# Kernel optimization log

Measured on AMD Instinct MI355X. Metric: run time of the kernel, lower is better.

## Reference

```python
import jax, jax.numpy as jnp
import numpy as np

SEQ, B, IN, H = 2048, 256, 64, 256


def setup_inputs() -> dict:
    key = jax.random.key(0)
    ks = jax.random.split(key, 5)
    s_in = 1.0 / np.sqrt(IN)
    s_h = 1.0 / np.sqrt(H)
    return {
        "x": jax.random.normal(ks[0], (SEQ, B, IN), jnp.float32),
        # combined gate weights, order (f, i, o, g)
        "Wx": jax.random.uniform(ks[1], (IN, 4 * H), jnp.float32, -s_in, s_in),
        "Wh": jax.random.uniform(ks[2], (H, 4 * H), jnp.float32, -s_h, s_h),
        "bx": jax.random.uniform(ks[3], (4 * H,), jnp.float32, -s_in, s_in),
        "bh": jax.random.uniform(ks[4], (4 * H,), jnp.float32, -s_h, s_h),
    }


def reference(x, Wx, Wh, bx, bh):
    # x: [T, B, IN]. Precompute input projections for all timesteps (one big GEMM).
    gx = jnp.einsum('tbi,ih->tbh', x, Wx) + bx + bh  # [T, B, 4H]
    h0 = jnp.zeros((x.shape[1], Wh.shape[0]), x.dtype)
    c0 = jnp.zeros_like(h0)

    def step(carry, gx_t):
        h, c = carry
        gates = gx_t + h @ Wh  # [B, 4H]
        f, i, o, g = jnp.split(gates, 4, axis=-1)
        c = jax.nn.sigmoid(f) * c + jax.nn.sigmoid(i) * jnp.tanh(g)
        h = jax.nn.sigmoid(o) * jnp.tanh(c)
        return (h, c), h

    (h, c), h_seq = jax.lax.scan(step, (h0, c0), gx)
    return h_seq, h, c
```

## Files before the change

kernel.cpp:

```cpp
#include <hip/hip_runtime.h>


#define T_SEQ 2048
#define B_SZ  256
#define IN_SZ 64
#define H_SZ  256
#define G4    1024
#define NKF   10
#define NCT   64
#define LDSK  648
#define FRAG_BYTES (NCT * NKF * 64 * 16)
#define BIAS_OFF   FRAG_BYTES
#define FLAGS_OFF  (FRAG_BYTES + 4096)
#define XBUF_OFF   (FRAG_BYTES + 8192)

typedef float f32x4 __attribute__((ext_vector_type(4)));
typedef short s16x8 __attribute__((ext_vector_type(8)));
typedef short s16x2 __attribute__((ext_vector_type(2)));
typedef unsigned u32x4 __attribute__((ext_vector_type(4)));

__device__ __forceinline__ short f2bf(float f) {
    unsigned u = __builtin_bit_cast(unsigned, f);
    u = u + 0x7fffu + ((u >> 16) & 1u);
    return (short)(u >> 16);
}
__device__ __forceinline__ float bf2f(short s) {
    return __builtin_bit_cast(float, ((unsigned)(unsigned short)s) << 16);
}
__device__ __forceinline__ float fsigmoid(float v) {
    return __builtin_amdgcn_rcpf(1.0f + __expf(-v));
}
__device__ __forceinline__ float ftanh(float v) {
    return 2.0f * __builtin_amdgcn_rcpf(1.0f + __expf(-2.0f * v)) - 1.0f;
}

__global__ void repack_kernel(const float* __restrict__ Wx,
                              const float* __restrict__ Wh,
                              const float* __restrict__ bx,
                              const float* __restrict__ bh,
                              s16x8* __restrict__ fragbuf,
                              float* __restrict__ bias) {
    const int blk  = blockIdx.x;
    const int lane = threadIdx.x;
    const int ct = blk / NKF;
    const int kf = blk - ct * NKF;
    const int n  = ct * 16 + (lane & 15);
    const int q  = lane >> 4;
    s16x8 frag;
#pragma unroll
    for (int j = 0; j < 8; ++j) {
        const int k = kf * 32 + q * 8 + j;
        const float v = (k < IN_SZ) ? Wx[k * G4 + n] : Wh[(k - IN_SZ) * G4 + n];
        frag[j] = f2bf(v);
    }
    fragbuf[blk * 64 + lane] = frag;
    if (blk < 16) {
        const int i = blk * 64 + lane;
        bias[i] = bx[i] + bh[i];
    }
}

__global__ void init_flags(unsigned* __restrict__ flags) {
    if (threadIdx.x < 32) flags[threadIdx.x] = 0u;
}

__global__ __launch_bounds__(512, 2) void lstm_persist(
        const float* __restrict__ x,
        const s16x8* __restrict__ fragbuf,
        const float* __restrict__ bias,
        float* __restrict__ out,
        unsigned* __restrict__ flags,
        unsigned* __restrict__ xbuf) {
    __shared__ short lds_a[2 * 16 * LDSK];

    const int tid  = threadIdx.x;
    const int lane = tid & 63;
    const int w    = tid >> 6;
    const int q    = lane >> 4;
    const int ln   = lane & 15;
    const int bid  = blockIdx.x;
    const int g    = bid >> 1;
    const int p    = bid & 1;
    const int peer = bid ^ 1;
    const int S    = g * 16;
    const int hb   = p * 8 + w;
    const int col  = hb * 16 + ln;

    for (int i = tid; i < 2 * 16 * LDSK; i += 512) lds_a[i] = 0;

    s16x8 wt[4][10];
#pragma unroll
    for (int ci = 0; ci < 4; ++ci) {
        const int ct = ci * 16 + hb;
#pragma unroll
        for (int j = 0; j < 10; ++j) {
            const int kf = (j < 2) ? j
                         : (j < 6 ? 2 + 4 * p + (j - 2)
                                  : 2 + 4 * (1 - p) + (j - 6));
            wt[ci][j] = fragbuf[(size_t)(ct * NKF + kf) * 64 + lane];
        }
    }
    float bs[4];
#pragma unroll
    for (int ci = 0; ci < 4; ++ci) bs[ci] = bias[(ci * 16 + hb) * 16 + ln];

    f32x4 cs = {0.f, 0.f, 0.f, 0.f};

    const int xrow = tid >> 5;
    const int xi   = (tid & 31) << 1;
    const float* xp0 = x + (size_t)(S + xrow) * IN_SZ + xi;
    float xv0 = xp0[0], xv1 = xp0[1];

    __syncthreads();

    for (int t = 0; t < T_SEQ; ++t) {
        const int cur = t & 1;
        short* L  = lds_a + cur * (16 * LDSK);
        short* Ln = lds_a + (1 - cur) * (16 * LDSK);

        {
            const short h0 = f2bf(xv0), h1 = f2bf(xv1);
            const short l0 = f2bf(xv0 - bf2f(h0));
            const short l1 = f2bf(xv1 - bf2f(h1));
            s16x2 hv = {h0, h1}, lv = {l0, l1};
            *reinterpret_cast<s16x2*>(&L[xrow * LDSK + xi])       = hv;
            *reinterpret_cast<s16x2*>(&L[xrow * LDSK + 320 + xi]) = lv;
        }
        {
            const int tn = (t + 1 < T_SEQ) ? t + 1 : t;
            const float* xp = xp0 + (size_t)tn * (B_SZ * IN_SZ);
            xv0 = xp[0]; xv1 = xp[1];
        }

        if (t > 0) {
            while (__hip_atomic_load(&flags[peer], __ATOMIC_RELAXED,
                                     __HIP_MEMORY_SCOPE_AGENT) < (unsigned)t) {
                __builtin_amdgcn_s_sleep(1);
            }
            __builtin_amdgcn_fence(__ATOMIC_ACQUIRE, "agent");
            const u32x4* ps = (const u32x4*)(xbuf
                              + (size_t)(peer * 2 + ((t - 1) & 1)) * 2048);
            const u32x4 v = ps[tid];
            const int colp = tid >> 2;
            const int cg   = 128 * (1 - p) + colp;
            const int m0   = (tid & 3) * 4;
#pragma unroll
            for (int e = 0; e < 4; ++e) {
                const unsigned u = v[e];
                const int m = m0 + e;
                L[m * LDSK + 64  + cg] = (short)(u & 0xffffu);
                L[m * LDSK + 384 + cg] = (short)(u >> 16);
            }
        }
        __syncthreads();

        f32x4 acc[4], acl[4];
#pragma unroll
        for (int ci = 0; ci < 4; ++ci) {
            acc[ci] = (f32x4){bs[ci], bs[ci], bs[ci], bs[ci]};
            acl[ci] = (f32x4){0.f, 0.f, 0.f, 0.f};
        }
#pragma unroll
        for (int j = 0; j < 10; ++j) {
            const int kf = (j < 2) ? j
                         : (j < 6 ? 2 + 4 * p + (j - 2)
                                  : 2 + 4 * (1 - p) + (j - 6));
            const s16x8 ah = *reinterpret_cast<const s16x8*>(
                                 &L[ln * LDSK + kf * 32 + q * 8]);
            const s16x8 al = *reinterpret_cast<const s16x8*>(
                                 &L[ln * LDSK + 320 + kf * 32 + q * 8]);
#pragma unroll
            for (int ci = 0; ci < 4; ++ci) {
                acc[ci] = __builtin_amdgcn_mfma_f32_16x16x32_bf16(ah, wt[ci][j], acc[ci], 0, 0, 0);
                acl[ci] = __builtin_amdgcn_mfma_f32_16x16x32_bf16(al, wt[ci][j], acl[ci], 0, 0, 0);
            }
        }
#pragma unroll
        for (int ci = 0; ci < 4; ++ci) acc[ci] += acl[ci];

        float* hs = out + (size_t)t * (B_SZ * H_SZ) + (size_t)S * H_SZ;
        unsigned* os = xbuf + (size_t)(bid * 2 + cur) * 2048;
        const bool last = (t == T_SEQ - 1);
        unsigned pu[4];
#pragma unroll
        for (int r = 0; r < 4; ++r) {
            const float fv = fsigmoid(acc[0][r]);
            const float iv = fsigmoid(acc[1][r]);
            const float ov = fsigmoid(acc[2][r]);
            const float gv = ftanh(acc[3][r]);
            const float cf = fv * cs[r] + iv * gv;
            cs[r] = cf;
            const float hv = ov * ftanh(cf);
            const int m = q * 4 + r;
            __builtin_nontemporal_store(hv, hs + m * H_SZ + col);
            const short hh = f2bf(hv);
            const short hl = f2bf(hv - bf2f(hh));
            Ln[m * LDSK + 64  + col] = hh;
            Ln[m * LDSK + 384 + col] = hl;
            pu[r] = ((unsigned)(unsigned short)hh)
                  | (((unsigned)(unsigned short)hl) << 16);
            if (last) {
                float* fin = out + (size_t)T_SEQ * B_SZ * H_SZ;
                fin[(S + m) * H_SZ + col] = hv;
                fin[B_SZ * H_SZ + (S + m) * H_SZ + col] = cf;
            }
        }
        {
            const int colp = w * 16 + ln;
            unsigned long long* od =
                (unsigned long long*)(os + colp * 16 + q * 4);
            const unsigned long long u01 =
                (unsigned long long)pu[0] | ((unsigned long long)pu[1] << 32);
            const unsigned long long u23 =
                (unsigned long long)pu[2] | ((unsigned long long)pu[3] << 32);
            __hip_atomic_store(&od[0], u01, __ATOMIC_RELAXED,
                               __HIP_MEMORY_SCOPE_AGENT);
            __hip_atomic_store(&od[1], u23, __ATOMIC_RELAXED,
                               __HIP_MEMORY_SCOPE_AGENT);
        }
        __syncthreads();
        if (tid == 0)
            __hip_atomic_store(&flags[bid], (unsigned)(t + 1),
                               __ATOMIC_RELEASE, __HIP_MEMORY_SCOPE_AGENT);
    }
}

extern "C" void kernel_launch(void* const* d_in, const int* in_sizes, int n_in,
                              void* d_out, int out_size, void* d_ws, size_t ws_size,
                              hipStream_t stream) {
    const float* x  = (const float*)d_in[0];
    const float* Wx = (const float*)d_in[1];
    const float* Wh = (const float*)d_in[2];
    const float* bx = (const float*)d_in[3];
    const float* bh = (const float*)d_in[4];
    float* out = (float*)d_out;

    s16x8*    fragbuf = (s16x8*)d_ws;
    float*    bias    = (float*)((char*)d_ws + BIAS_OFF);
    unsigned* flags   = (unsigned*)((char*)d_ws + FLAGS_OFF);
    unsigned* xbuf    = (unsigned*)((char*)d_ws + XBUF_OFF);

    repack_kernel<<<NCT * NKF, 64, 0, stream>>>(Wx, Wh, bx, bh, fragbuf, bias);
    init_flags<<<1, 64, 0, stream>>>(flags);
    lstm_persist<<<32, 512, 0, stream>>>(x, fragbuf, bias, out, flags, xbuf);
}
```

Measured before the change: 12.57 ms.

## Overlap peer hidden-state exchange with local MFMA work using per-wave flags

Restructures the per-timestep cross-block exchange. Each wave publishes its h slice in MFMA-fragment layout and bumps a per-wave counter with fetch_add, so the peer can load those fragments straight into registers instead of going through LDS plus a barrier. The local K-fragments (x and own-half h) are computed before waiting on the peer, so the wait overlaps with MFMA work. The LDS layout switches to an XOR swizzle to avoid bank conflicts, and the x staging for step t+1 moves to the end of step t. The relaxed loads after the spin and the counter-based readiness check rely on subtle memory-ordering assumptions, which is a correctness risk.

```diff
diff --git a/kernel.cpp b/kernel.cpp
--- a/kernel.cpp
+++ b/kernel.cpp
@@ -8,16 +8,19 @@
 #define G4    1024
 #define NKF   10
 #define NCT   64
-#define LDSK  648
 #define FRAG_BYTES (NCT * NKF * 64 * 16)
 #define BIAS_OFF   FRAG_BYTES
 #define FLAGS_OFF  (FRAG_BYTES + 4096)
 #define XBUF_OFF   (FRAG_BYTES + 8192)
+#define ROW_B   768
+#define BUF_B   (16 * ROW_B)
+#define PUB_OFF (2 * BUF_B)
 
 typedef float f32x4 __attribute__((ext_vector_type(4)));
 typedef short s16x8 __attribute__((ext_vector_type(8)));
 typedef short s16x2 __attribute__((ext_vector_type(2)));
-typedef unsigned u32x4 __attribute__((ext_vector_type(4)));
+typedef unsigned long long u64;
+typedef u64 u64x2 __attribute__((ext_vector_type(2)));
 
 __device__ __forceinline__ short f2bf(float f) {
     unsigned u = __builtin_bit_cast(unsigned, f);
@@ -32,6 +35,9 @@
 }
 __device__ __forceinline__ float ftanh(float v) {
     return 2.0f * __builtin_amdgcn_rcpf(1.0f + __expf(-2.0f * v)) - 1.0f;
+}
+__device__ __forceinline__ short* aptr(char* lds, int buf, int row, int off) {
+    return (short*)(lds + buf * BUF_B + row * ROW_B + (off ^ ((row & 7) << 4)));
 }
 
 __global__ void repack_kernel(const float* __restrict__ Wx,
@@ -70,8 +76,8 @@
         const float* __restrict__ bias,
         float* __restrict__ out,
         unsigned* __restrict__ flags,
-        unsigned* __restrict__ xbuf) {
-    __shared__ short lds_a[2 * 16 * LDSK];
+        char* __restrict__ xbuf) {
+    __shared__ char lds[PUB_OFF + 8704];
 
     const int tid  = threadIdx.x;
     const int lane = tid & 63;
@@ -85,8 +91,10 @@
     const int S    = g * 16;
     const int hb   = p * 8 + w;
     const int col  = hb * 16 + ln;
-
-    for (int i = tid; i < 2 * 16 * LDSK; i += 512) lds_a[i] = 0;
+    const int colp = w * 16 + ln;
+
+    for (int i = tid; i < (PUB_OFF + 8704) / 4; i += 512)
+        ((int*)lds)[i] = 0;
 
     s16x8 wt[4][10];
 #pragma unroll
@@ -111,48 +119,40 @@
     const float* xp0 = x + (size_t)(S + xrow) * IN_SZ + xi;
     float xv0 = xp0[0], xv1 = xp0[1];
 
+    {
+        const short h0 = f2bf(xv0), h1 = f2bf(xv1);
+        const short l0 = f2bf(xv0 - bf2f(h0));
+        const short l1 = f2bf(xv1 - bf2f(h1));
+        *(s16x2*)aptr(lds, 0, xrow, xi * 2)       = (s16x2){h0, h1};
+        *(s16x2*)aptr(lds, 0, xrow, 384 + xi * 2) = (s16x2){l0, l1};
+    }
+    {
+        const float* xp = xp0 + (size_t)(B_SZ * IN_SZ);
+        xv0 = xp[0]; xv1 = xp[1];
+    }
+    unsigned* psw = (unsigned*)(lds + PUB_OFF) + w * 272;
+    unsigned rdyflag = 0;
+
     __syncthreads();
 
     for (int t = 0; t < T_SEQ; ++t) {
         const int cur = t & 1;
-        short* L  = lds_a + cur * (16 * LDSK);
-        short* Ln = lds_a + (1 - cur) * (16 * LDSK);
-
-        {
-            const short h0 = f2bf(xv0), h1 = f2bf(xv1);
-            const short l0 = f2bf(xv0 - bf2f(h0));
-            const short l1 = f2bf(xv1 - bf2f(h1));
-            s16x2 hv = {h0, h1}, lv = {l0, l1};
-            *reinterpret_cast<s16x2*>(&L[xrow * LDSK + xi])       = hv;
-            *reinterpret_cast<s16x2*>(&L[xrow * LDSK + 320 + xi]) = lv;
-        }
-        {
-            const int tn = (t + 1 < T_SEQ) ? t + 1 : t;
-            const float* xp = xp0 + (size_t)tn * (B_SZ * IN_SZ);
-            xv0 = xp[0]; xv1 = xp[1];
-        }
-
-        if (t > 0) {
-            while (__hip_atomic_load(&flags[peer], __ATOMIC_RELAXED,
-                                     __HIP_MEMORY_SCOPE_AGENT) < (unsigned)t) {
-                __builtin_amdgcn_s_sleep(1);
-            }
-            __builtin_amdgcn_fence(__ATOMIC_ACQUIRE, "agent");
-            const u32x4* ps = (const u32x4*)(xbuf
-                              + (size_t)(peer * 2 + ((t - 1) & 1)) * 2048);
-            const u32x4 v = ps[tid];
-            const int colp = tid >> 2;
-            const int cg   = 128 * (1 - p) + colp;
-            const int m0   = (tid & 3) * 4;
-#pragma unroll
-            for (int e = 0; e < 4; ++e) {
-                const unsigned u = v[e];
-                const int m = m0 + e;
-                L[m * LDSK + 64  + cg] = (short)(u & 0xffffu);
-                L[m * LDSK + 384 + cg] = (short)(u >> 16);
-            }
-        }
-        __syncthreads();
+        char* mySlot = xbuf + (size_t)bid  * 16384 + (size_t)cur * 8192;
+        char* pSlot  = xbuf + (size_t)peer * 16384 + (size_t)((t - 1) & 1) * 8192;
+        const unsigned tgt = 8u * (unsigned)t;
+        bool ready = (t > 0) && (rdyflag >= tgt);
+
+        u64 ph[8], pl[8];
+        if (ready) {
+#pragma unroll
+            for (int jj = 0; jj < 4; ++jj) {
+                const int off = ln * 256 + jj * 64 + q * 16;
+                ph[2*jj]   = __hip_atomic_load((const u64*)(pSlot + off),       __ATOMIC_RELAXED, __HIP_MEMORY_SCOPE_AGENT);
+                ph[2*jj+1] = __hip_atomic_load((const u64*)(pSlot + off + 8),   __ATOMIC_RELAXED, __HIP_MEMORY_SCOPE_AGENT);
+                pl[2*jj]   = __hip_atomic_load((const u64*)(pSlot + 4096 + off),__ATOMIC_RELAXED, __HIP_MEMORY_SCOPE_AGENT);
+                pl[2*jj+1] = __hip_atomic_load((const u64*)(pSlot + 4104 + off),__ATOMIC_RELAXED, __HIP_MEMORY_SCOPE_AGENT);
+            }
+        }
 
         f32x4 acc[4], acl[4];
 #pragma unroll
@@ -161,27 +161,47 @@
             acl[ci] = (f32x4){0.f, 0.f, 0.f, 0.f};
         }
 #pragma unroll
-        for (int j = 0; j < 10; ++j) {
-            const int kf = (j < 2) ? j
-                         : (j < 6 ? 2 + 4 * p + (j - 2)
-                                  : 2 + 4 * (1 - p) + (j - 6));
-            const s16x8 ah = *reinterpret_cast<const s16x8*>(
-                                 &L[ln * LDSK + kf * 32 + q * 8]);
-            const s16x8 al = *reinterpret_cast<const s16x8*>(
-                                 &L[ln * LDSK + 320 + kf * 32 + q * 8]);
+        for (int j = 0; j < 6; ++j) {
+            const s16x8 ah = *(const s16x8*)aptr(lds, cur, ln, j * 64 + q * 16);
+            const s16x8 al = *(const s16x8*)aptr(lds, cur, ln, 384 + j * 64 + q * 16);
 #pragma unroll
             for (int ci = 0; ci < 4; ++ci) {
                 acc[ci] = __builtin_amdgcn_mfma_f32_16x16x32_bf16(ah, wt[ci][j], acc[ci], 0, 0, 0);
                 acl[ci] = __builtin_amdgcn_mfma_f32_16x16x32_bf16(al, wt[ci][j], acl[ci], 0, 0, 0);
             }
         }
+
+        if (t > 0) {
+            if (!ready) {
+                while (__hip_atomic_load(&flags[peer], __ATOMIC_RELAXED,
+                                         __HIP_MEMORY_SCOPE_AGENT) < tgt)
+                    __builtin_amdgcn_s_sleep(1);
+                asm volatile("" ::: "memory");
+#pragma unroll
+                for (int jj = 0; jj < 4; ++jj) {
+                    const int off = ln * 256 + jj * 64 + q * 16;
+                    ph[2*jj]   = __hip_atomic_load((const u64*)(pSlot + off),       __ATOMIC_RELAXED, __HIP_MEMORY_SCOPE_AGENT);
+                    ph[2*jj+1] = __hip_atomic_load((const u64*)(pSlot + off + 8),   __ATOMIC_RELAXED, __HIP_MEMORY_SCOPE_AGENT);
+                    pl[2*jj]   = __hip_atomic_load((const u64*)(pSlot + 4096 + off),__ATOMIC_RELAXED, __HIP_MEMORY_SCOPE_AGENT);
+                    pl[2*jj+1] = __hip_atomic_load((const u64*)(pSlot + 4104 + off),__ATOMIC_RELAXED, __HIP_MEMORY_SCOPE_AGENT);
+                }
+            }
+#pragma unroll
+            for (int jj = 0; jj < 4; ++jj) {
+                const s16x8 ah = __builtin_bit_cast(s16x8, (u64x2){ph[2*jj], ph[2*jj+1]});
+                const s16x8 al = __builtin_bit_cast(s16x8, (u64x2){pl[2*jj], pl[2*jj+1]});
+#pragma unroll
+                for (int ci = 0; ci < 4; ++ci) {
+                    acc[ci] = __builtin_amdgcn_mfma_f32_16x16x32_bf16(ah, wt[ci][6 + jj], acc[ci], 0, 0, 0);
+                    acl[ci] = __builtin_amdgcn_mfma_f32_16x16x32_bf16(al, wt[ci][6 + jj], acl[ci], 0, 0, 0);
+                }
+            }
+        }
 #pragma unroll
         for (int ci = 0; ci < 4; ++ci) acc[ci] += acl[ci];
 
-        float* hs = out + (size_t)t * (B_SZ * H_SZ) + (size_t)S * H_SZ;
-        unsigned* os = xbuf + (size_t)(bid * 2 + cur) * 2048;
         const bool last = (t == T_SEQ - 1);
-        unsigned pu[4];
+        float hvr[4]; float cfr[4]; unsigned pu[4];
 #pragma unroll
         for (int r = 0; r < 4; ++r) {
             const float fv = fsigmoid(acc[0][r]);
@@ -189,39 +209,63 @@
             const float ov = fsigmoid(acc[2][r]);
             const float gv = ftanh(acc[3][r]);
             const float cf = fv * cs[r] + iv * gv;
-            cs[r] = cf;
+            cs[r] = cf; cfr[r] = cf;
             const float hv = ov * ftanh(cf);
-            const int m = q * 4 + r;
-            __builtin_nontemporal_store(hv, hs + m * H_SZ + col);
+            hvr[r] = hv;
             const short hh = f2bf(hv);
             const short hl = f2bf(hv - bf2f(hh));
-            Ln[m * LDSK + 64  + col] = hh;
-            Ln[m * LDSK + 384 + col] = hl;
             pu[r] = ((unsigned)(unsigned short)hh)
                   | (((unsigned)(unsigned short)hl) << 16);
+        }
+
+#pragma unroll
+        for (int r = 0; r < 4; ++r) psw[ln * 17 + q * 4 + r] = pu[r];
+        {
+            const int m2 = lane & 15;
+            const int cc = lane >> 4;
+            const unsigned t0 = psw[(cc * 4 + 0) * 17 + m2];
+            const unsigned t1 = psw[(cc * 4 + 1) * 17 + m2];
+            const unsigned t2 = psw[(cc * 4 + 2) * 17 + m2];
+            const unsigned t3 = psw[(cc * 4 + 3) * 17 + m2];
+            const u64 hi64 = (u64)(t0 & 0xffffu) | ((u64)(t1 & 0xffffu) << 16)
+                           | ((u64)(t2 & 0xffffu) << 32) | ((u64)(t3 & 0xffffu) << 48);
+            const u64 lo64 = (u64)(t0 >> 16) | ((u64)(t1 >> 16) << 16)
+                           | ((u64)(t2 >> 16) << 32) | ((u64)(t3 >> 16) << 48);
+            const int off = m2 * 256 + w * 32 + cc * 8;
+            __hip_atomic_store((u64*)(mySlot + off),        hi64, __ATOMIC_RELAXED, __HIP_MEMORY_SCOPE_AGENT);
+            __hip_atomic_store((u64*)(mySlot + 4096 + off), lo64, __ATOMIC_RELAXED, __HIP_MEMORY_SCOPE_AGENT);
+        }
+        asm volatile("s_waitcnt vmcnt(0)" ::: "memory");
+        if (lane == 0)
+            (void)__hip_atomic_fetch_add(&flags[bid], 1u, __ATOMIC_RELAXED,
+                                         __HIP_MEMORY_SCOPE_AGENT);
+
+        float* hs = out + (size_t)t * (B_SZ * H_SZ) + (size_t)S * H_SZ;
+#pragma unroll
+        for (int r = 0; r < 4; ++r) {
+            const int m = q * 4 + r;
+            __builtin_nontemporal_store(hvr[r], hs + m * H_SZ + col);
+            *aptr(lds, cur ^ 1, m, 128 + colp * 2) = (short)(pu[r] & 0xffffu);
+            *aptr(lds, cur ^ 1, m, 512 + colp * 2) = (short)(pu[r] >> 16);
             if (last) {
                 float* fin = out + (size_t)T_SEQ * B_SZ * H_SZ;
-                fin[(S + m) * H_SZ + col] = hv;
-                fin[B_SZ * H_SZ + (S + m) * H_SZ + col] = cf;
+                fin[(S + m) * H_SZ + col] = hvr[r];
+                fin[B_SZ * H_SZ + (S + m) * H_SZ + col] = cfr[r];
             }
         }
         {
-            const int colp = w * 16 + ln;
-            unsigned long long* od =
-                (unsigned long long*)(os + colp * 16 + q * 4);
-            const unsigned long long u01 =
-                (unsigned long long)pu[0] | ((unsigned long long)pu[1] << 32);
-            const unsigned long long u23 =
-                (unsigned long long)pu[2] | ((unsigned long long)pu[3] << 32);
-            __hip_atomic_store(&od[0], u01, __ATOMIC_RELAXED,
-                               __HIP_MEMORY_SCOPE_AGENT);
-            __hip_atomic_store(&od[1], u23, __ATOMIC_RELAXED,
-                               __HIP_MEMORY_SCOPE_AGENT);
-        }
+            const short h0 = f2bf(xv0), h1 = f2bf(xv1);
+            const short l0 = f2bf(xv0 - bf2f(h0));
+            const short l1 = f2bf(xv1 - bf2f(h1));
+            *(s16x2*)aptr(lds, cur ^ 1, xrow, xi * 2)       = (s16x2){h0, h1};
+            *(s16x2*)aptr(lds, cur ^ 1, xrow, 384 + xi * 2) = (s16x2){l0, l1};
+            const int tn = (t + 2 < T_SEQ) ? t + 2 : T_SEQ - 1;
+            const float* xp = xp0 + (size_t)tn * (B_SZ * IN_SZ);
+            xv0 = xp[0]; xv1 = xp[1];
+        }
+        rdyflag = __hip_atomic_load(&flags[peer], __ATOMIC_RELAXED,
+                                    __HIP_MEMORY_SCOPE_AGENT);
         __syncthreads();
-        if (tid == 0)
-            __hip_atomic_store(&flags[bid], (unsigned)(t + 1),
-                               __ATOMIC_RELEASE, __HIP_MEMORY_SCOPE_AGENT);
     }
 }
 
@@ -238,7 +282,7 @@
     s16x8*    fragbuf = (s16x8*)d_ws;
     float*    bias    = (float*)((char*)d_ws + BIAS_OFF);
     unsigned* flags   = (unsigned*)((char*)d_ws + FLAGS_OFF);
-    unsigned* xbuf    = (unsigned*)((char*)d_ws + XBUF_OFF);
+    char*     xbuf    = (char*)d_ws + XBUF_OFF;
 
     repack_kernel<<<NCT * NKF, 64, 0, stream>>>(Wx, Wh, bx, bh, fragbuf, bias);
     init_flags<<<1, 64, 0, stream>>>(flags);
```

After: 23.93 ms. +90.4%, slower.
